# Performance work log

Hardware: AMD Instinct MI355X
Metric: run time of the kernel (lower is better)

The kernel has to match this reference:

```python
import jax, jax.numpy as jnp
import numpy as np

MAX_WAVELENGTH = 10000.0
NUM_HEADS = 15
NUM_KV_HEADS = 5
HEAD_DIM = 64


def apply_rope(x, positions):
    """RoPE: x [B, L, H, D], positions [B, L] (int)."""
    d_half = x.shape[-1] // 2
    x = x.astype(jnp.float32)
    freq_exponents = (2.0 / x.shape[-1]) * jnp.arange(d_half, dtype=jnp.float32)
    timescale = MAX_WAVELENGTH ** freq_exponents  # [d_half]
    radians = positions[..., None].astype(jnp.float32) / timescale  # [B, L, d_half]
    radians = radians[..., None, :]  # [B, L, 1, d_half]
    sin, cos = jnp.sin(radians), jnp.cos(radians)
    x1, x2 = x[..., :d_half], x[..., d_half:]
    return jnp.concatenate([x1 * cos - x2 * sin, x2 * cos + x1 * sin], axis=-1)


def setup_inputs() -> dict:
    key = jax.random.key(0)
    k1, k2, k3, k4 = jax.random.split(key, 4)
    B, L = 2, 2048
    query_states = jax.random.normal(k1, (B, L, NUM_HEADS, HEAD_DIM), dtype=jnp.float32)
    key_states = jax.random.normal(k2, (B, L, NUM_KV_HEADS, HEAD_DIM), dtype=jnp.float32)
    value_states = jax.random.normal(k3, (B, L, NUM_KV_HEADS, HEAD_DIM), dtype=jnp.float32)
    positions = jnp.sort(jax.random.randint(k4, (B, L), 0, L, dtype=jnp.int32), axis=-1)
    # Causal (prefix-LM) boolean mask [B, L, L]
    attention_mask = jnp.broadcast_to(jnp.tril(jnp.ones((L, L), dtype=bool)), (B, L, L))
    return {
        "query_states": query_states,
        "key_states": key_states,
        "value_states": value_states,
        "positions": positions,
        "attention_mask": attention_mask,
    }


def reference(query_states, key_states, value_states, positions, attention_mask):
    B, L = query_states.shape[0], query_states.shape[1]
    groups = NUM_HEADS // NUM_KV_HEADS  # 3

    # RoPE on Q and K (eager, per original module)
    q = apply_rope(query_states, positions)  # [B, L, 15, 64] fp32
    k = apply_rope(key_states, positions)    # [B, L, 5, 64]  fp32

    # GQA expansion: [B, L, Kv, D] -> [B, L, Kv*groups, D]
    k = jnp.repeat(k, groups, axis=2)
    v = jnp.repeat(value_states, groups, axis=2).astype(jnp.float32)

    # Scores in fp32: [B, H, Lq, Lk]
    scores = jnp.einsum("bqhd,bkhd->bhqk", q, k) * (HEAD_DIM ** -0.5)
    big_neg = jnp.finfo(jnp.float32).min
    scores = jnp.where(attention_mask[:, None, :, :], scores, big_neg)
    probs = jax.nn.softmax(scores, axis=-1)

    out = jnp.einsum("bhqk,bkhd->bqhd", probs, v)  # [B, L, H, D]
    return out.reshape(B, L, NUM_HEADS * HEAD_DIM)  # [B, L, 960]
```

## Files before the change

### kernel.cpp

```cpp
#include <hip/hip_runtime.h>
#include <math.h>

#define NB 2
#define NL 2048
#define NHQ 15
#define NKV 5
#define HD 64
#define NT 32
#define GRP 3
#define PST 72
#define NG 16
#define SLOTF 2080

typedef __attribute__((ext_vector_type(8))) short short8;
typedef __attribute__((ext_vector_type(4))) float floatx4;

#define ROPE_C 0.28782313662425575f
#define QSCALE 0.18033688011116016f

__device__ __forceinline__ ushort f2bf(float x) {
    unsigned u = __builtin_bit_cast(unsigned, x);
    u = (u + 0x7FFFu + ((u >> 16) & 1u)) >> 16;
    return (ushort)u;
}
__device__ __forceinline__ unsigned pk2(float a, float b) {
    unsigned ua = __builtin_bit_cast(unsigned, a) + 0x8000u;
    unsigned ub = __builtin_bit_cast(unsigned, b) + 0x8000u;
    return __builtin_amdgcn_perm(ub, ua, 0x07060302u);
}
__device__ __forceinline__ void async16(ushort* lds, const ushort* g) {
    __builtin_amdgcn_global_load_lds(
        (const __attribute__((address_space(1))) unsigned int*)g,
        (__attribute__((address_space(3))) unsigned int*)lds, 16, 0, 0);
}

union U8  { short8 v; ushort u[8]; };
union F8  { float4 f4[2]; float f[8]; };

__global__ __launch_bounds__(256)
void prep_kv(const float* __restrict__ K, const float* __restrict__ V,
             const int* __restrict__ pos, ushort* __restrict__ Kr,
             ushort* __restrict__ Vr) {
    __shared__ float Vs[64][65];
    const int bid = blockIdx.x, t = threadIdx.x;
    if (bid < NB * NKV * NT) {
        int b = bid / (NKV * NT), rem = bid % (NKV * NT);
        int h = rem / NT, k0 = (rem % NT) * 64;
        int j = t >> 2, c0 = t & 3;
        int row = k0 + j;
        const float* src = K + ((size_t)((b * NL + row) * NKV + h)) * HD;
        int db = c0 * 8;
        F8 x1, x2;
        x1.f4[0] = *(const float4*)&src[db];
        x1.f4[1] = *(const float4*)&src[db + 4];
        x2.f4[0] = *(const float4*)&src[db + 32];
        x2.f4[1] = *(const float4*)&src[db + 36];
        float ps = (float)pos[b * NL + row];
        U8 lo, hi;
#pragma unroll
        for (int i = 0; i < 8; ++i) {
            float inv = __expf((float)(db + i) * -ROPE_C);
            float sn, cs; __sincosf(ps * inv, &sn, &cs);
            lo.u[i] = f2bf(x1.f[i] * cs - x2.f[i] * sn);
            hi.u[i] = f2bf(x2.f[i] * cs + x1.f[i] * sn);
        }
        ushort* dst = Kr + (size_t)bid * 4096;
        *(short8*)&dst[(j * 8 + (c0 ^ (j & 7))) * 8]       = lo.v;
        *(short8*)&dst[(j * 8 + ((c0 + 4) ^ (j & 7))) * 8] = hi.v;
    } else {
        int vb = bid - NB * NKV * NT;
        int b = vb / (NKV * NT), rem = vb % (NKV * NT);
        int h = rem / NT, k0 = (rem % NT) * 64;
#pragma unroll
        for (int it = 0; it < 4; ++it) {
            int e = t + it * 256;
            int j = e >> 4, d4 = (e & 15) * 4;
            *(float4*)&Vs[j][d4] =
                *(const float4*)&V[((size_t)((b * NL + k0 + j) * NKV + h)) * HD + d4];
        }
        __syncthreads();
        ushort* dst = Vr + (size_t)vb * 4096;
#pragma unroll
        for (int it = 0; it < 2; ++it) {
            int o = t + it * 256;
            int d = o >> 3, c = o & 7, j0 = c * 8;
            U8 r;
#pragma unroll
            for (int k = 0; k < 8; ++k) r.u[k] = f2bf(Vs[j0 + k][d]);
            *(short8*)&dst[(d * 8 + (c ^ (d & 7))) * 8] = r.v;
        }
    }
}

__global__ __launch_bounds__(256, 4)
void attn_partial(const float* __restrict__ Q, const ushort* __restrict__ Kr,
                  const ushort* __restrict__ Vr, const int* __restrict__ pos,
                  float* __restrict__ Pw, float* __restrict__ out,
                  int CH, int TOT) {
    __shared__ __align__(16) ushort Kb[4096];
    __shared__ __align__(16) ushort Vb[4096];
    __shared__ __align__(16) ushort Pb[4][2][16 * PST];

    const int t = threadIdx.x;
    const int w = t >> 6, lane = t & 63;
    const int l16 = lane & 15, quad = lane >> 4;
    const int h = blockIdx.y, b = blockIdx.z;
    const int kvh = h / GRP;
    const int fidx = TOT - 1 - (int)blockIdx.x;

    int g = 0, chunk = fidx;
    for (; g < NG; ++g) {
        int ncg = (2 * g + 2 + CH - 1) / CH;
        if (chunk < ncg) break;
        chunk -= ncg;
    }
    const int ntg = 2 * g + 2;
    const int nc  = (ntg + CH - 1) / CH;
    const int kb0 = chunk * CH;
    int kb1 = kb0 + CH; if (kb1 > ntg) kb1 = ntg;
    const int qi = 4 * g + w;
    const int ntw = (qi >> 1) + 1;
    const int r0 = qi * 32;

    short8 Qa[2][2];
#pragma unroll
    for (int rf = 0; rf < 2; ++rf) {
        int row = r0 + rf * 16 + l16;
        const float* src = Q + ((size_t)((b * NL + row) * NHQ + h)) * HD;
        int db = quad * 8;
        F8 x1, x2;
        x1.f4[0] = *(const float4*)&src[db];
        x1.f4[1] = *(const float4*)&src[db + 4];
        x2.f4[0] = *(const float4*)&src[db + 32];
        x2.f4[1] = *(const float4*)&src[db + 36];
        float ps = (float)pos[b * NL + row];
        union { short8 v; unsigned u[4]; } lo, hi;
#pragma unroll
        for (int i = 0; i < 8; i += 2) {
            float inv0 = __expf((float)(db + i) * -ROPE_C);
            float inv1 = __expf((float)(db + i + 1) * -ROPE_C);
            float sn0, cs0, sn1, cs1;
            __sincosf(ps * inv0, &sn0, &cs0);
            __sincosf(ps * inv1, &sn1, &cs1);
            float l0 = (x1.f[i] * cs0 - x2.f[i] * sn0) * QSCALE;
            float l1 = (x1.f[i + 1] * cs1 - x2.f[i + 1] * sn1) * QSCALE;
            float h0 = (x2.f[i] * cs0 + x1.f[i] * sn0) * QSCALE;
            float h1 = (x2.f[i + 1] * cs1 + x1.f[i + 1] * sn1) * QSCALE;
            lo.u[i >> 1] = pk2(l0, l1);
            hi.u[i >> 1] = pk2(h0, h1);
        }
        Qa[rf][0] = lo.v;
        Qa[rf][1] = hi.v;
    }

    floatx4 O[2][4];
    float lsum[2] = {0.f, 0.f};
#pragma unroll
    for (int rf = 0; rf < 2; ++rf)
#pragma unroll
        for (int d = 0; d < 4; ++d) O[rf][d] = (floatx4){0.f, 0.f, 0.f, 0.f};

    const ushort* Kt0 = Kr + (size_t)((b * NKV + kvh) * NT) * 4096;
    const ushort* Vt0 = Vr + (size_t)((b * NKV + kvh) * NT) * 4096;
    const int swz8[2] = { ((quad)     ^ (l16 & 7)) * 8,
                          ((quad + 4) ^ (l16 & 7)) * 8 };
    const int so = w * 1024;

    for (int kb = kb0; kb < kb1; ++kb) {
        {
            const ushort* Kt = Kt0 + (size_t)kb * 4096;
            const ushort* Vt = Vt0 + (size_t)kb * 4096;
            async16(&Kb[so],       Kt + so + lane * 8);
            async16(&Kb[so + 512], Kt + so + 512 + lane * 8);
            async16(&Vb[so],       Vt + so + lane * 8);
            async16(&Vb[so + 512], Vt + so + 512 + lane * 8);
        }
        __syncthreads();

        if (kb < ntw) {
            floatx4 S[2][4];
#pragma unroll
            for (int rf = 0; rf < 2; ++rf)
#pragma unroll
                for (int c = 0; c < 4; ++c) S[rf][c] = (floatx4){0.f, 0.f, 0.f, 0.f};
#pragma unroll
            for (int s = 0; s < 2; ++s)
#pragma unroll
                for (int c = 0; c < 4; ++c) {
                    short8 kfv = *(const short8*)&Kb[(c * 16 + l16) * 64 + swz8[s]];
                    S[0][c] = __builtin_amdgcn_mfma_f32_16x16x32_bf16(kfv, Qa[0][s], S[0][c], 0, 0, 0);
                    S[1][c] = __builtin_amdgcn_mfma_f32_16x16x32_bf16(kfv, Qa[1][s], S[1][c], 0, 0, 0);
                }

            if (kb == ntw - 1) {
#pragma unroll
                for (int rf = 0; rf < 2; ++rf) {
                    int qrow = r0 + rf * 16 + l16;
                    float acc = 0.f;
#pragma unroll
                    for (int c = 0; c < 4; ++c) {
                        float pv[4];
#pragma unroll
                        for (int r = 0; r < 4; ++r) {
                            int key = kb * 64 + c * 16 + quad * 4 + r;
                            float sv = S[rf][c][r];
                            if (key > qrow) sv = -1e30f;
                            pv[r] = exp2f(sv);
                            acc += pv[r];
                        }
                        *(uint2*)&Pb[w][rf][l16 * PST + c * 16 + quad * 4] =
                            make_uint2(pk2(pv[0], pv[1]), pk2(pv[2], pv[3]));
                    }
                    lsum[rf] += acc;
                }
            } else {
#pragma unroll
                for (int rf = 0; rf < 2; ++rf) {
                    float acc = 0.f;
#pragma unroll
                    for (int c = 0; c < 4; ++c) {
                        float pv[4];
#pragma unroll
                        for (int r = 0; r < 4; ++r) {
                            pv[r] = exp2f(S[rf][c][r]);
                            acc += pv[r];
                        }
                        *(uint2*)&Pb[w][rf][l16 * PST + c * 16 + quad * 4] =
                            make_uint2(pk2(pv[0], pv[1]), pk2(pv[2], pv[3]));
                    }
                    lsum[rf] += acc;
                }
            }

#pragma unroll
            for (int s = 0; s < 2; ++s) {
                short8 pf0 = *(const short8*)&Pb[w][0][l16 * PST + s * 32 + quad * 8];
                short8 pf1 = *(const short8*)&Pb[w][1][l16 * PST + s * 32 + quad * 8];
#pragma unroll
                for (int d = 0; d < 4; ++d) {
                    short8 vfv = *(const short8*)&Vb[(d * 16 + l16) * 64 + swz8[s]];
                    O[0][d] = __builtin_amdgcn_mfma_f32_16x16x32_bf16(vfv, pf0, O[0][d], 0, 0, 0);
                    O[1][d] = __builtin_amdgcn_mfma_f32_16x16x32_bf16(vfv, pf1, O[1][d], 0, 0, 0);
                }
            }
        }
        __syncthreads();
    }

    if (nc == 1) {
#pragma unroll
        for (int rf = 0; rf < 2; ++rf) {
            float ls = lsum[rf];
            ls += __shfl_xor(ls, 16, 64);
            ls += __shfl_xor(ls, 32, 64);
            float rinv = 1.0f / ls;
            int qrow = r0 + rf * 16 + l16;
            float* op = out + (size_t)(b * NL + qrow) * (NHQ * HD) + h * HD;
#pragma unroll
            for (int d = 0; d < 4; ++d) {
                float4 o = make_float4(O[rf][d][0] * rinv, O[rf][d][1] * rinv,
                                       O[rf][d][2] * rinv, O[rf][d][3] * rinv);
                *(float4*)&op[d * 16 + quad * 4] = o;
            }
        }
    } else {
        float* slot = Pw + (((size_t)(b * NHQ + h) * TOT + fidx) * 4 + w) * SLOTF;
#pragma unroll
        for (int rf = 0; rf < 2; ++rf) {
#pragma unroll
            for (int d = 0; d < 4; ++d) {
                float4 o = make_float4(O[rf][d][0], O[rf][d][1], O[rf][d][2], O[rf][d][3]);
                *(float4*)&slot[(rf * 16 + l16) * 64 + d * 16 + quad * 4] = o;
            }
            float ls = lsum[rf];
            ls += __shfl_xor(ls, 16, 64);
            ls += __shfl_xor(ls, 32, 64);
            if (quad == 0) slot[2048 + rf * 16 + l16] = ls;
        }
    }
}

__global__ __launch_bounds__(256)
void combine(const float* __restrict__ Pw, float* __restrict__ out,
             int CH, int TOT, int qi0) {
    __shared__ float ls[32];
    const int qi = qi0 + blockIdx.x;
    const int bh = blockIdx.y;
    const int b = bh / NHQ, h = bh % NHQ;
    const int g = qi >> 2, w = qi & 3;
    const int nch = (2 * g + 2 + CH - 1) / CH;
    int pfx = 0;
    for (int gg = 0; gg < g; ++gg) pfx += (2 * gg + 2 + CH - 1) / CH;
    const float* base = Pw + (((size_t)bh * TOT + pfx) * 4 + w) * SLOTF;

    const int t = threadIdx.x;
    const int rl = t >> 3, d0 = (t & 7) * 8;
    float a[8];
#pragma unroll
    for (int k = 0; k < 8; ++k) a[k] = 0.f;
    float lacc = 0.f;
    for (int c = 0; c < nch; ++c) {
        const float* pb = base + (size_t)c * 4 * SLOTF;
        float4 x0 = *(const float4*)&pb[rl * 64 + d0];
        float4 x1 = *(const float4*)&pb[rl * 64 + d0 + 4];
        a[0] += x0.x; a[1] += x0.y; a[2] += x0.z; a[3] += x0.w;
        a[4] += x1.x; a[5] += x1.y; a[6] += x1.z; a[7] += x1.w;
        if (t < 32) lacc += pb[2048 + t];
    }
    if (t < 32) ls[t] = lacc;
    __syncthreads();
    float rinv = 1.0f / ls[rl];
    float* op = out + (size_t)(b * NL + qi * 32 + rl) * (NHQ * HD) + h * HD + d0;
    *(float4*)&op[0] = make_float4(a[0] * rinv, a[1] * rinv, a[2] * rinv, a[3] * rinv);
    *(float4*)&op[4] = make_float4(a[4] * rinv, a[5] * rinv, a[6] * rinv, a[7] * rinv);
}

extern "C" void kernel_launch(void* const* d_in, const int* in_sizes, int n_in,
                              void* d_out, int out_size, void* d_ws, size_t ws_size,
                              hipStream_t stream) {
    const float* Q   = (const float*)d_in[0];
    const float* K   = (const float*)d_in[1];
    const float* V   = (const float*)d_in[2];
    const int*   pos = (const int*)d_in[3];
    ushort* Kr = (ushort*)d_ws;
    ushort* Vr = Kr + (size_t)NB * NKV * NT * 4096;
    float*  Pw = (float*)(Vr + (size_t)NB * NKV * NT * 4096);
    float*  out = (float*)d_out;
    const size_t prepBytes = (size_t)2 * NB * NKV * NT * 4096 * sizeof(ushort);

    int CH = 32, TOT = NG;
    const int ladder[3] = {4, 8, 16};
    for (int i = 0; i < 3; ++i) {
        int ch = ladder[i], tot = 0;
        for (int gq = 0; gq < NG; ++gq) tot += (2 * gq + 2 + ch - 1) / ch;
        size_t need = prepBytes + (size_t)NB * NHQ * tot * 4 * SLOTF * sizeof(float);
        if (need <= ws_size) { CH = ch; TOT = tot; break; }
    }

    prep_kv<<<2 * NB * NKV * NT, 256, 0, stream>>>(K, V, pos, Kr, Vr);
    dim3 grid(TOT, NHQ, NB);
    attn_partial<<<grid, 256, 0, stream>>>(Q, Kr, Vr, pos, Pw, out, CH, TOT);
    int qi0 = 2 * CH;
    if (qi0 < 64)
        combine<<<dim3(64 - qi0, NB * NHQ), 256, 0, stream>>>(Pw, out, CH, TOT, qi0);
}
```

Before: 149.9 us.

## Replace split-K partial/combine with paired-tile flash kernel and double-buffered KV

```diff
diff --git a/kernel.cpp b/kernel.cpp
--- a/kernel.cpp
+++ b/kernel.cpp
@@ -9,8 +9,6 @@
 #define NT 32
 #define GRP 3
 #define PST 72
-#define NG 16
-#define SLOTF 2080
 
 typedef __attribute__((ext_vector_type(8))) short short8;
 typedef __attribute__((ext_vector_type(4))) float floatx4;
@@ -92,73 +90,26 @@
     }
 }
 
-__global__ __launch_bounds__(256, 4)
-void attn_partial(const float* __restrict__ Q, const ushort* __restrict__ Kr,
-                  const ushort* __restrict__ Vr, const int* __restrict__ pos,
-                  float* __restrict__ Pw, float* __restrict__ out,
-                  int CH, int TOT) {
-    __shared__ __align__(16) ushort Kb[4096];
-    __shared__ __align__(16) ushort Vb[4096];
+__global__ __launch_bounds__(256, 1)
+void attn_flash(const float* __restrict__ Q, const ushort* __restrict__ Kr,
+                const ushort* __restrict__ Vr, const int* __restrict__ pos,
+                float* __restrict__ out) {
+    __shared__ __align__(16) ushort Kb[2][4096];
+    __shared__ __align__(16) ushort Vb[2][4096];
     __shared__ __align__(16) ushort Pb[4][2][16 * PST];
 
     const int t = threadIdx.x;
     const int w = t >> 6, lane = t & 63;
     const int l16 = lane & 15, quad = lane >> 4;
-    const int h = blockIdx.y, b = blockIdx.z;
-    const int kvh = h / GRP;
-    const int fidx = TOT - 1 - (int)blockIdx.x;
-
-    int g = 0, chunk = fidx;
-    for (; g < NG; ++g) {
-        int ncg = (2 * g + 2 + CH - 1) / CH;
-        if (chunk < ncg) break;
-        chunk -= ncg;
-    }
-    const int ntg = 2 * g + 2;
-    const int nc  = (ntg + CH - 1) / CH;
-    const int kb0 = chunk * CH;
-    int kb1 = kb0 + CH; if (kb1 > ntg) kb1 = ntg;
-    const int qi = 4 * g + w;
-    const int ntw = (qi >> 1) + 1;
-    const int r0 = qi * 32;
-
-    short8 Qa[2][2];
-#pragma unroll
-    for (int rf = 0; rf < 2; ++rf) {
-        int row = r0 + rf * 16 + l16;
-        const float* src = Q + ((size_t)((b * NL + row) * NHQ + h)) * HD;
-        int db = quad * 8;
-        F8 x1, x2;
-        x1.f4[0] = *(const float4*)&src[db];
-        x1.f4[1] = *(const float4*)&src[db + 4];
-        x2.f4[0] = *(const float4*)&src[db + 32];
-        x2.f4[1] = *(const float4*)&src[db + 36];
-        float ps = (float)pos[b * NL + row];
-        union { short8 v; unsigned u[4]; } lo, hi;
-#pragma unroll
-        for (int i = 0; i < 8; i += 2) {
-            float inv0 = __expf((float)(db + i) * -ROPE_C);
-            float inv1 = __expf((float)(db + i + 1) * -ROPE_C);
-            float sn0, cs0, sn1, cs1;
-            __sincosf(ps * inv0, &sn0, &cs0);
-            __sincosf(ps * inv1, &sn1, &cs1);
-            float l0 = (x1.f[i] * cs0 - x2.f[i] * sn0) * QSCALE;
-            float l1 = (x1.f[i + 1] * cs1 - x2.f[i + 1] * sn1) * QSCALE;
-            float h0 = (x2.f[i] * cs0 + x1.f[i] * sn0) * QSCALE;
-            float h1 = (x2.f[i + 1] * cs1 + x1.f[i + 1] * sn1) * QSCALE;
-            lo.u[i >> 1] = pk2(l0, l1);
-            hi.u[i >> 1] = pk2(h0, h1);
-        }
-        Qa[rf][0] = lo.v;
-        Qa[rf][1] = hi.v;
-    }
-
-    floatx4 O[2][4];
-    float lsum[2] = {0.f, 0.f};
-#pragma unroll
-    for (int rf = 0; rf < 2; ++rf)
-#pragma unroll
-        for (int d = 0; d < 4; ++d) O[rf][d] = (floatx4){0.f, 0.f, 0.f, 0.f};
+
+    const int bid  = blockIdx.x;
+    const int work = (bid & 7) * 30 + (bid >> 3);
+    const int pi = work & 7;
+    int rem = work >> 3;
+    const int hg = rem % 3; rem /= 3;
+    const int kvh = rem % 5;
+    const int b = rem / 5;
+    const int h = kvh * GRP + hg;
 
     const ushort* Kt0 = Kr + (size_t)((b * NKV + kvh) * NT) * 4096;
     const ushort* Vt0 = Vr + (size_t)((b * NKV + kvh) * NT) * 4096;
@@ -166,88 +117,142 @@
                           ((quad + 4) ^ (l16 & 7)) * 8 };
     const int so = w * 1024;
 
-    for (int kb = kb0; kb < kb1; ++kb) {
-        {
-            const ushort* Kt = Kt0 + (size_t)kb * 4096;
-            const ushort* Vt = Vt0 + (size_t)kb * 4096;
-            async16(&Kb[so],       Kt + so + lane * 8);
-            async16(&Kb[so + 512], Kt + so + 512 + lane * 8);
-            async16(&Vb[so],       Vt + so + lane * 8);
-            async16(&Vb[so + 512], Vt + so + 512 + lane * 8);
-        }
+    for (int ph = 0; ph < 2; ++ph) {
+        const int g   = ph ? (15 - pi) : pi;
+        const int qi  = 4 * g + w;
+        const int ntb = 2 * g + 2;
+        const int ntw = (qi >> 1) + 1;
+        const int r0  = qi * 32;
+
+        async16(&Kb[0][so],       Kt0 + so + lane * 8);
+        async16(&Kb[0][so + 512], Kt0 + so + 512 + lane * 8);
+        async16(&Vb[0][so],       Vt0 + so + lane * 8);
+        async16(&Vb[0][so + 512], Vt0 + so + 512 + lane * 8);
+
+        short8 Qa[2][2];
+#pragma unroll
+        for (int rf = 0; rf < 2; ++rf) {
+            int row = r0 + rf * 16 + l16;
+            const float* src = Q + ((size_t)((b * NL + row) * NHQ + h)) * HD;
+            int db = quad * 8;
+            F8 x1, x2;
+            x1.f4[0] = *(const float4*)&src[db];
+            x1.f4[1] = *(const float4*)&src[db + 4];
+            x2.f4[0] = *(const float4*)&src[db + 32];
+            x2.f4[1] = *(const float4*)&src[db + 36];
+            float ps = (float)pos[b * NL + row];
+            union { short8 v; unsigned u[4]; } lo, hi;
+#pragma unroll
+            for (int i = 0; i < 8; i += 2) {
+                float inv0 = __expf((float)(db + i) * -ROPE_C);
+                float inv1 = __expf((float)(db + i + 1) * -ROPE_C);
+                float sn0, cs0, sn1, cs1;
+                __sincosf(ps * inv0, &sn0, &cs0);
+                __sincosf(ps * inv1, &sn1, &cs1);
+                float lo0 = (x1.f[i] * cs0 - x2.f[i] * sn0) * QSCALE;
+                float lo1 = (x1.f[i + 1] * cs1 - x2.f[i + 1] * sn1) * QSCALE;
+                float hi0 = (x2.f[i] * cs0 + x1.f[i] * sn0) * QSCALE;
+                float hi1 = (x2.f[i + 1] * cs1 + x1.f[i + 1] * sn1) * QSCALE;
+                lo.u[i >> 1] = pk2(lo0, lo1);
+                hi.u[i >> 1] = pk2(hi0, hi1);
+            }
+            Qa[rf][0] = lo.v;
+            Qa[rf][1] = hi.v;
+        }
+
+        floatx4 O[2][4];
+        float lsum[2] = {0.f, 0.f};
+#pragma unroll
+        for (int rf = 0; rf < 2; ++rf)
+#pragma unroll
+            for (int d = 0; d < 4; ++d) O[rf][d] = (floatx4){0.f, 0.f, 0.f, 0.f};
+
         __syncthreads();
 
-        if (kb < ntw) {
-            floatx4 S[2][4];
-#pragma unroll
-            for (int rf = 0; rf < 2; ++rf)
-#pragma unroll
-                for (int c = 0; c < 4; ++c) S[rf][c] = (floatx4){0.f, 0.f, 0.f, 0.f};
-#pragma unroll
-            for (int s = 0; s < 2; ++s)
-#pragma unroll
-                for (int c = 0; c < 4; ++c) {
-                    short8 kfv = *(const short8*)&Kb[(c * 16 + l16) * 64 + swz8[s]];
-                    S[0][c] = __builtin_amdgcn_mfma_f32_16x16x32_bf16(kfv, Qa[0][s], S[0][c], 0, 0, 0);
-                    S[1][c] = __builtin_amdgcn_mfma_f32_16x16x32_bf16(kfv, Qa[1][s], S[1][c], 0, 0, 0);
+        int cur = 0;
+        for (int kb = 0; kb < ntb; ++kb) {
+            if (kb + 1 < ntb) {
+                const ushort* Kt = Kt0 + (size_t)(kb + 1) * 4096;
+                const ushort* Vt = Vt0 + (size_t)(kb + 1) * 4096;
+                const int nx = cur ^ 1;
+                async16(&Kb[nx][so],       Kt + so + lane * 8);
+                async16(&Kb[nx][so + 512], Kt + so + 512 + lane * 8);
+                async16(&Vb[nx][so],       Vt + so + lane * 8);
+                async16(&Vb[nx][so + 512], Vt + so + 512 + lane * 8);
+            }
+
+            if (kb < ntw) {
+                floatx4 S[2][4];
+#pragma unroll
+                for (int rf = 0; rf < 2; ++rf)
+#pragma unroll
+                    for (int c = 0; c < 4; ++c) S[rf][c] = (floatx4){0.f, 0.f, 0.f, 0.f};
+#pragma unroll
+                for (int s = 0; s < 2; ++s)
+#pragma unroll
+                    for (int c = 0; c < 4; ++c) {
+                        short8 kfv = *(const short8*)&Kb[cur][(c * 16 + l16) * 64 + swz8[s]];
+                        S[0][c] = __builtin_amdgcn_mfma_f32_16x16x32_bf16(kfv, Qa[0][s], S[0][c], 0, 0, 0);
+                        S[1][c] = __builtin_amdgcn_mfma_f32_16x16x32_bf16(kfv, Qa[1][s], S[1][c], 0, 0, 0);
+                    }
+
+                if (kb == ntw - 1) {
+#pragma unroll
+                    for (int rf = 0; rf < 2; ++rf) {
+                        int qrow = r0 + rf * 16 + l16;
+                        float acc = 0.f;
+#pragma unroll
+                        for (int c = 0; c < 4; ++c) {
+                            float pv[4];
+#pragma unroll
+                            for (int r = 0; r < 4; ++r) {
+                                int key = kb * 64 + c * 16 + quad * 4 + r;
+                                float sv = S[rf][c][r];
+                                if (key > qrow) sv = -1e30f;
+                                pv[r] = exp2f(sv);
+                                acc += pv[r];
+                            }
+                            *(uint2*)&Pb[w][rf][l16 * PST + c * 16 + quad * 4] =
+                                make_uint2(pk2(pv[0], pv[1]), pk2(pv[2], pv[3]));
+                        }
+                        lsum[rf] += acc;
+                    }
+                } else {
+#pragma unroll
+                    for (int rf = 0; rf < 2; ++rf) {
+                        float acc = 0.f;
+#pragma unroll
+                        for (int c = 0; c < 4; ++c) {
+                            float pv[4];
+#pragma unroll
+                            for (int r = 0; r < 4; ++r) {
+                                pv[r] = exp2f(S[rf][c][r]);
+                                acc += pv[r];
+                            }
+                            *(uint2*)&Pb[w][rf][l16 * PST + c * 16 + quad * 4] =
+                                make_uint2(pk2(pv[0], pv[1]), pk2(pv[2], pv[3]));
+                        }
+                        lsum[rf] += acc;
+                    }
                 }
 
-            if (kb == ntw - 1) {
-#pragma unroll
-                for (int rf = 0; rf < 2; ++rf) {
-                    int qrow = r0 + rf * 16 + l16;
-                    float acc = 0.f;
-#pragma unroll
-                    for (int c = 0; c < 4; ++c) {
-                        float pv[4];
-#pragma unroll
-                        for (int r = 0; r < 4; ++r) {
-                            int key = kb * 64 + c * 16 + quad * 4 + r;
-                            float sv = S[rf][c][r];
-                            if (key > qrow) sv = -1e30f;
-                            pv[r] = exp2f(sv);
-                            acc += pv[r];
-                        }
-                        *(uint2*)&Pb[w][rf][l16 * PST + c * 16 + quad * 4] =
-                            make_uint2(pk2(pv[0], pv[1]), pk2(pv[2], pv[3]));
-                    }
-                    lsum[rf] += acc;
+#pragma unroll
+                for (int s = 0; s < 2; ++s) {
+                    short8 pf0 = *(const short8*)&Pb[w][0][l16 * PST + s * 32 + quad * 8];
+                    short8 pf1 = *(const short8*)&Pb[w][1][l16 * PST + s * 32 + quad * 8];
+#pragma unroll
+                    for (int d = 0; d < 4; ++d) {
+                        short8 vfv = *(const short8*)&Vb[cur][(d * 16 + l16) * 64 + swz8[s]];
+                        O[0][d] = __builtin_amdgcn_mfma_f32_16x16x32_bf16(vfv, pf0, O[0][d], 0, 0, 0);
+                        O[1][d] = __builtin_amdgcn_mfma_f32_16x16x32_bf16(vfv, pf1, O[1][d], 0, 0, 0);
+                    }
                 }
-            } else {
-#pragma unroll
-                for (int rf = 0; rf < 2; ++rf) {
-                    float acc = 0.f;
-#pragma unroll
-                    for (int c = 0; c < 4; ++c) {
-                        float pv[4];
-#pragma unroll
-                        for (int r = 0; r < 4; ++r) {
-                            pv[r] = exp2f(S[rf][c][r]);
-                            acc += pv[r];
-                        }
-                        *(uint2*)&Pb[w][rf][l16 * PST + c * 16 + quad * 4] =
-                            make_uint2(pk2(pv[0], pv[1]), pk2(pv[2], pv[3]));
-                    }
-                    lsum[rf] += acc;
-                }
-            }
-
-#pragma unroll
-            for (int s = 0; s < 2; ++s) {
-                short8 pf0 = *(const short8*)&Pb[w][0][l16 * PST + s * 32 + quad * 8];
-                short8 pf1 = *(const short8*)&Pb[w][1][l16 * PST + s * 32 + quad * 8];
-#pragma unroll
-                for (int d = 0; d < 4; ++d) {
-                    short8 vfv = *(const short8*)&Vb[(d * 16 + l16) * 64 + swz8[s]];
-                    O[0][d] = __builtin_amdgcn_mfma_f32_16x16x32_bf16(vfv, pf0, O[0][d], 0, 0, 0);
-                    O[1][d] = __builtin_amdgcn_mfma_f32_16x16x32_bf16(vfv, pf1, O[1][d], 0, 0, 0);
-                }
-            }
-        }
-        __syncthreads();
-    }
-
-    if (nc == 1) {
+            }
+
+            __syncthreads();
+            cur ^= 1;
+        }
+
 #pragma unroll
         for (int rf = 0; rf < 2; ++rf) {
             float ls = lsum[rf];
@@ -263,56 +268,7 @@
                 *(float4*)&op[d * 16 + quad * 4] = o;
             }
         }
-    } else {
-        float* slot = Pw + (((size_t)(b * NHQ + h) * TOT + fidx) * 4 + w) * SLOTF;
-#pragma unroll
-        for (int rf = 0; rf < 2; ++rf) {
-#pragma unroll
-            for (int d = 0; d < 4; ++d) {
-                float4 o = make_float4(O[rf][d][0], O[rf][d][1], O[rf][d][2], O[rf][d][3]);
-                *(float4*)&slot[(rf * 16 + l16) * 64 + d * 16 + quad * 4] = o;
-            }
-            float ls = lsum[rf];
-            ls += __shfl_xor(ls, 16, 64);
-            ls += __shfl_xor(ls, 32, 64);
-            if (quad == 0) slot[2048 + rf * 16 + l16] = ls;
-        }
     }
-}
-
-__global__ __launch_bounds__(256)
-void combine(const float* __restrict__ Pw, float* __restrict__ out,
-             int CH, int TOT, int qi0) {
-    __shared__ float ls[32];
-    const int qi = qi0 + blockIdx.x;
-    const int bh = blockIdx.y;
-    const int b = bh / NHQ, h = bh % NHQ;
-    const int g = qi >> 2, w = qi & 3;
-    const int nch = (2 * g + 2 + CH - 1) / CH;
-    int pfx = 0;
-    for (int gg = 0; gg < g; ++gg) pfx += (2 * gg + 2 + CH - 1) / CH;
-    const float* base = Pw + (((size_t)bh * TOT + pfx) * 4 + w) * SLOTF;
-
-    const int t = threadIdx.x;
-    const int rl = t >> 3, d0 = (t & 7) * 8;
-    float a[8];
-#pragma unroll
-    for (int k = 0; k < 8; ++k) a[k] = 0.f;
-    float lacc = 0.f;
-    for (int c = 0; c < nch; ++c) {
-        const float* pb = base + (size_t)c * 4 * SLOTF;
-        float4 x0 = *(const float4*)&pb[rl * 64 + d0];
-        float4 x1 = *(const float4*)&pb[rl * 64 + d0 + 4];
-        a[0] += x0.x; a[1] += x0.y; a[2] += x0.z; a[3] += x0.w;
-        a[4] += x1.x; a[5] += x1.y; a[6] += x1.z; a[7] += x1.w;
-        if (t < 32) lacc += pb[2048 + t];
-    }
-    if (t < 32) ls[t] = lacc;
-    __syncthreads();
-    float rinv = 1.0f / ls[rl];
-    float* op = out + (size_t)(b * NL + qi * 32 + rl) * (NHQ * HD) + h * HD + d0;
-    *(float4*)&op[0] = make_float4(a[0] * rinv, a[1] * rinv, a[2] * rinv, a[3] * rinv);
-    *(float4*)&op[4] = make_float4(a[4] * rinv, a[5] * rinv, a[6] * rinv, a[7] * rinv);
 }
 
 extern "C" void kernel_launch(void* const* d_in, const int* in_sizes, int n_in,
@@ -324,23 +280,8 @@
     const int*   pos = (const int*)d_in[3];
     ushort* Kr = (ushort*)d_ws;
     ushort* Vr = Kr + (size_t)NB * NKV * NT * 4096;
-    float*  Pw = (float*)(Vr + (size_t)NB * NKV * NT * 4096);
     float*  out = (float*)d_out;
-    const size_t prepBytes = (size_t)2 * NB * NKV * NT * 4096 * sizeof(ushort);
-
-    int CH = 32, TOT = NG;
-    const int ladder[3] = {4, 8, 16};
-    for (int i = 0; i < 3; ++i) {
-        int ch = ladder[i], tot = 0;
-        for (int gq = 0; gq < NG; ++gq) tot += (2 * gq + 2 + ch - 1) / ch;
-        size_t need = prepBytes + (size_t)NB * NHQ * tot * 4 * SLOTF * sizeof(float);
-        if (need <= ws_size) { CH = ch; TOT = tot; break; }
-    }
 
     prep_kv<<<2 * NB * NKV * NT, 256, 0, stream>>>(K, V, pos, Kr, Vr);
-    dim3 grid(TOT, NHQ, NB);
-    attn_partial<<<grid, 256, 0, stream>>>(Q, Kr, Vr, pos, Pw, out, CH, TOT);
-    int qi0 = 2 * CH;
-    if (qi0 < 64)
-        combine<<<dim3(64 - qi0, NB * NHQ), 256, 0, stream>>>(Pw, out, CH, TOT, qi0);
-}
+    attn_flash<<<NB * NHQ * 8, 256, 0, stream>>>(Q, Kr, Vr, pos, out);
+}
```

Result: no change. 150.8 us (+0.6%).
